# Optimization experiments

Hardware: AMD Instinct MI355X
Metric: run time of the kernel (lower is better)

Reference implementation:

```python
import jax, jax.numpy as jnp
import numpy as np

WS = 8  # window size
NH = 6  # num heads


def _rel_pos_index(ws):
    coords = jnp.stack(jnp.meshgrid(jnp.arange(ws), jnp.arange(ws), indexing='ij'))  # (2, ws, ws)
    cf = coords.reshape(2, -1)                      # (2, ws*ws)
    rel = cf[:, :, None] - cf[:, None, :]           # (2, ws2, ws2)
    return (rel[0] + ws - 1) * (2 * ws - 1) + (rel[1] + ws - 1)  # (ws2, ws2) int


def setup_inputs() -> dict:
    key = jax.random.key(0)
    k1, k2, k3, k4, k5 = jax.random.split(key, 5)
    B, H, W, C = 4, 256, 256, 192
    dim = C
    x = jax.random.normal(k1, (B, H * W, C), dtype=jnp.float32)
    qkv_w = jax.random.normal(k2, (3 * dim, dim), dtype=jnp.float32) * (dim ** -0.5)
    proj_w = jax.random.normal(k3, (dim, dim), dtype=jnp.float32) * (dim ** -0.5)
    proj_b = jax.random.normal(k4, (dim,), dtype=jnp.float32) * 0.01
    rpb_table = jax.random.normal(k5, ((2 * WS - 1) ** 2, NH), dtype=jnp.float32) * 0.02
    return {"x": x, "qkv_w": qkv_w, "proj_w": proj_w, "proj_b": proj_b,
            "rpb_table": rpb_table, "H": H, "W": W}


def reference(x, qkv_w, proj_w, proj_b, rpb_table, H, W):
    B, L, C = x.shape
    ws, nh = WS, NH
    hd = C // nh
    scale = hd ** -0.5
    ws2 = ws * ws

    pad_r = (ws - W % ws) % ws
    pad_b = (ws - H % ws) % ws
    Hp, Wp = H + pad_b, W + pad_r
    xi = x.reshape(B, H, W, C)
    if pad_r > 0 or pad_b > 0:
        xi = jnp.pad(xi, ((0, 0), (0, pad_b), (0, pad_r), (0, 0)))

    # window partition -> (nW, ws2, C)
    win = xi.reshape(B, Hp // ws, ws, Wp // ws, ws, C)
    win = win.transpose(0, 1, 3, 2, 4, 5).reshape(-1, ws2, C)

    # qkv projection (no bias)
    qkv = (win @ qkv_w.T).reshape(-1, ws2, 3, nh, hd)
    q = qkv[:, :, 0].transpose(0, 2, 1, 3) * scale  # (nW, nh, ws2, hd)
    k = qkv[:, :, 1].transpose(0, 2, 1, 3)
    v = qkv[:, :, 2].transpose(0, 2, 1, 3)

    attn = jnp.einsum('nhqd,nhkd->nhqk', q, k)      # (nW, nh, ws2, ws2)
    bias = rpb_table[_rel_pos_index(ws)]            # (ws2, ws2, nh)
    attn = attn + bias.transpose(2, 0, 1)[None]
    attn = jax.nn.softmax(attn, axis=-1)

    out = jnp.einsum('nhqk,nhkd->nhqd', attn, v)    # (nW, nh, ws2, hd)
    out = out.transpose(0, 2, 1, 3).reshape(-1, ws2, C)
    out = out @ proj_w.T + proj_b

    # window reverse
    xo = out.reshape(B, Hp // ws, Wp // ws, ws, ws, C)
    xo = xo.transpose(0, 1, 3, 2, 4, 5).reshape(B, Hp, Wp, C)
    if pad_r > 0 or pad_b > 0:
        xo = xo[:, :H, :W, :]
    return xo.reshape(B, H * W, C)
```

## Files before the change

kernel.cpp:

```cpp
#include <hip/hip_runtime.h>

typedef _Float16 f16;
typedef _Float16 f16x8 __attribute__((ext_vector_type(8)));
typedef _Float16 f16x4 __attribute__((ext_vector_type(4)));
typedef __fp16 h16x2 __attribute__((ext_vector_type(2)));
typedef float f32x4 __attribute__((ext_vector_type(4)));

constexpr int HDIM = 256, WDIM = 256, C_ = 192, NH_ = 6;
constexpr float SCALE = 0.17677669529663687f;
constexpr int XP = 200;

#define SCHED_FENCE() __builtin_amdgcn_sched_barrier(0)

constexpr size_t OFF_WQ   = 0;
constexpr size_t OFF_WP   = 221184;
constexpr size_t OFF_BIAS = 294912;

__global__ __launch_bounds__(256) void prep_kernel(const float* __restrict__ qkv_w,
                                                   const float* __restrict__ proj_w,
                                                   const float* __restrict__ rpb,
                                                   f16* __restrict__ wqp, f16* __restrict__ wpp,
                                                   f16* __restrict__ biasp) {
    int i = blockIdx.x * 256 + threadIdx.x;
    if (i < 13824) {
        int lane = i & 63, rest = i >> 6;
        int ks = rest % 6; rest /= 6;
        int dt = rest & 1; rest >>= 1;
        int c = rest % 3, w = rest / 3;
        int l15 = lane & 15, lg = lane >> 4;
        int row = c * 192 + w * 32 + dt * 16 + l15;
        int col = ks * 32 + lg * 8;
#pragma unroll
        for (int j = 0; j < 8; ++j) wqp[(size_t)i * 8 + j] = (f16)qkv_w[row * 192 + col + j];
    } else if (i < 18432) {
        int g = i - 13824;
        int lane = g & 63, rest = g >> 6;
        int ks = rest % 6; rest /= 6;
        int nt = rest & 1, w = rest >> 1;
        int l15 = lane & 15, lg = lane >> 4;
        int row = w * 32 + nt * 16 + l15;
        int col = ks * 32 + lg * 8;
#pragma unroll
        for (int j = 0; j < 8; ++j) wpp[(size_t)g * 8 + j] = (f16)proj_w[row * 192 + col + j];
    } else if (i < 24576) {
        int g = i - 18432;
        int lane = g & 63;
        int kt = (g >> 6) & 3, qt = (g >> 8) & 3, h = g >> 10;
        int q = qt * 16 + (lane & 15);
#pragma unroll
        for (int j = 0; j < 4; ++j) {
            int k = kt * 16 + (lane >> 4) * 4 + j;
            int dy = (q >> 3) - (k >> 3) + 7;
            int dx = (q & 7) - (k & 7) + 7;
            biasp[(size_t)g * 4 + j] = (f16)rpb[(dy * 15 + dx) * NH_ + h];
        }
    }
}

__global__ __launch_bounds__(128, 2) void fused_kernel(const float* __restrict__ x,
                                                       const f16* __restrict__ wqp,
                                                       const f16* __restrict__ wpp,
                                                       const float* __restrict__ pb,
                                                       const f16* __restrict__ biasp,
                                                       float* __restrict__ out) {
    __shared__ f16 xlds[64 * XP];
    const int tid = threadIdx.x;
    const int v = tid >> 6;
    const int lane = tid & 63;
    const int l15 = lane & 15, lg = lane >> 4;
    const int win = blockIdx.x;
    const int b = win >> 10, wy = (win >> 5) & 31, wx = win & 31;

#pragma unroll
    for (int it = 0; it < 24; ++it) {
        int u = tid + it * 128;
        int row = u / 48, c4 = u - row * 48;
        int gy = wy * 8 + (row >> 3), gx = wx * 8 + (row & 7);
        float4 vv = *((const float4*)(x + ((size_t)((b * HDIM + gy) * WDIM + gx)) * C_ + c4 * 4));
        h16x2 p0 = __builtin_amdgcn_cvt_pkrtz(vv.x, vv.y);
        h16x2 p1 = __builtin_amdgcn_cvt_pkrtz(vv.z, vv.w);
        f16x4 o4;
        o4[0] = (f16)p0[0]; o4[1] = (f16)p0[1]; o4[2] = (f16)p1[0]; o4[3] = (f16)p1[1];
        *((f16x4*)(xlds + row * XP + c4 * 4)) = o4;
    }
    SCHED_FENCE();
    __syncthreads();

    f16x4 oreg[3][4][2];

#pragma unroll
    for (int hh = 0; hh < 3; ++hh) {
        const int head = v * 3 + hh;
        const f16x8* wqb   = (const f16x8*)wqp + (size_t)head * 36 * 64 + lane;
        const f16x4* bbase = (const f16x4*)biasp + (size_t)head * 16 * 64 + lane;
        SCHED_FENCE();

        f16x4 qf[2][4], kf[2][4];
        {
            f32x4 aq[2][4], ak[2][4];
#pragma unroll
            for (int ii = 0; ii < 4; ++ii)
#pragma unroll
                for (int jj = 0; jj < 2; ++jj) {
                    f32x4 z = {0.f, 0.f, 0.f, 0.f};
                    aq[jj][ii] = z; ak[jj][ii] = z;
                }
#pragma unroll
            for (int ks = 0; ks < 6; ++ks) {
                f16x8 Wq0 = wqb[(size_t)(     ks) * 64], Wq1 = wqb[(size_t)( 6 + ks) * 64];
                f16x8 Wk0 = wqb[(size_t)(12 + ks) * 64], Wk1 = wqb[(size_t)(18 + ks) * 64];
#pragma unroll
                for (int tt = 0; tt < 4; ++tt) {
                    f16x8 xt = *((const f16x8*)(xlds + (tt * 16 + l15) * XP + ks * 32 + lg * 8));
                    aq[0][tt] = __builtin_amdgcn_mfma_f32_16x16x32_f16(Wq0, xt, aq[0][tt], 0, 0, 0);
                    aq[1][tt] = __builtin_amdgcn_mfma_f32_16x16x32_f16(Wq1, xt, aq[1][tt], 0, 0, 0);
                    ak[0][tt] = __builtin_amdgcn_mfma_f32_16x16x32_f16(Wk0, xt, ak[0][tt], 0, 0, 0);
                    ak[1][tt] = __builtin_amdgcn_mfma_f32_16x16x32_f16(Wk1, xt, ak[1][tt], 0, 0, 0);
                }
            }
#pragma unroll
            for (int dt = 0; dt < 2; ++dt)
#pragma unroll
                for (int tt = 0; tt < 4; ++tt)
#pragma unroll
                    for (int ii = 0; ii < 4; ++ii) {
                        qf[dt][tt][ii] = (f16)(aq[dt][tt][ii] * SCALE);
                        kf[dt][tt][ii] = (f16)(ak[dt][tt][ii]);
                    }
        }
        SCHED_FENCE();

        f16x4 vf[4][2];
        {
            f32x4 av[4][2];
#pragma unroll
            for (int ii = 0; ii < 4; ++ii)
#pragma unroll
                for (int jj = 0; jj < 2; ++jj) {
                    f32x4 z = {0.f, 0.f, 0.f, 0.f};
                    av[ii][jj] = z;
                }
#pragma unroll
            for (int ks = 0; ks < 6; ++ks) {
                f16x8 Wv0 = wqb[(size_t)(24 + ks) * 64], Wv1 = wqb[(size_t)(30 + ks) * 64];
#pragma unroll
                for (int tt = 0; tt < 4; ++tt) {
                    f16x8 xt = *((const f16x8*)(xlds + (tt * 16 + l15) * XP + ks * 32 + lg * 8));
                    av[tt][0] = __builtin_amdgcn_mfma_f32_16x16x32_f16(xt, Wv0, av[tt][0], 0, 0, 0);
                    av[tt][1] = __builtin_amdgcn_mfma_f32_16x16x32_f16(xt, Wv1, av[tt][1], 0, 0, 0);
                }
            }
#pragma unroll
            for (int tt = 0; tt < 4; ++tt)
#pragma unroll
                for (int dt = 0; dt < 2; ++dt)
#pragma unroll
                    for (int ii = 0; ii < 4; ++ii)
                        vf[tt][dt][ii] = (f16)(av[tt][dt][ii]);
        }
        SCHED_FENCE();

#pragma unroll
        for (int qt = 0; qt < 4; ++qt) {
            f16x4 bq[4];
#pragma unroll
            for (int kt = 0; kt < 4; ++kt)
                bq[kt] = bbase[(size_t)(qt * 4 + kt) * 64];
            f32x4 s[4];
#pragma unroll
            for (int kt = 0; kt < 4; ++kt) {
                f32x4 z = {0.f, 0.f, 0.f, 0.f};
                s[kt] = __builtin_amdgcn_mfma_f32_16x16x16f16(kf[0][kt], qf[0][qt], z, 0, 0, 0);
                s[kt] = __builtin_amdgcn_mfma_f32_16x16x16f16(kf[1][kt], qf[1][qt], s[kt], 0, 0, 0);
            }
#pragma unroll
            for (int kt = 0; kt < 4; ++kt)
#pragma unroll
                for (int ii = 0; ii < 4; ++ii) s[kt][ii] += (float)bq[kt][ii];

            float m = s[0][0];
#pragma unroll
            for (int kt = 0; kt < 4; ++kt)
#pragma unroll
                for (int ii = 0; ii < 4; ++ii) m = fmaxf(m, s[kt][ii]);
            m = fmaxf(m, __shfl_xor(m, 16));
            m = fmaxf(m, __shfl_xor(m, 32));
            float sum = 0.f;
            f16x4 pa[4];
#pragma unroll
            for (int kt = 0; kt < 4; ++kt)
#pragma unroll
                for (int ii = 0; ii < 4; ++ii) {
                    float e = __expf(s[kt][ii] - m);
                    sum += e;
                    pa[kt][ii] = (f16)e;
                }
            sum += __shfl_xor(sum, 16);
            sum += __shfl_xor(sum, 32);
            const float rq = 1.0f / sum;

#pragma unroll
            for (int dt = 0; dt < 2; ++dt) {
                f32x4 z = {0.f, 0.f, 0.f, 0.f};
                f32x4 o0 = __builtin_amdgcn_mfma_f32_16x16x16f16(vf[0][dt], pa[0], z, 0, 0, 0);
                o0 = __builtin_amdgcn_mfma_f32_16x16x16f16(vf[1][dt], pa[1], o0, 0, 0, 0);
                f32x4 o1 = __builtin_amdgcn_mfma_f32_16x16x16f16(vf[2][dt], pa[2], z, 0, 0, 0);
                o1 = __builtin_amdgcn_mfma_f32_16x16x16f16(vf[3][dt], pa[3], o1, 0, 0, 0);
                f32x4 o = o0 + o1;
                f16x4 ov;
#pragma unroll
                for (int ii = 0; ii < 4; ++ii) ov[ii] = (f16)(o[ii] * rq);
                oreg[hh][qt][dt] = ov;
            }
        }
    }
    SCHED_FENCE();
    __syncthreads();

#pragma unroll
    for (int hh = 0; hh < 3; ++hh) {
        const int head = v * 3 + hh;
#pragma unroll
        for (int qt = 0; qt < 4; ++qt)
#pragma unroll
            for (int dt = 0; dt < 2; ++dt)
                *((f16x4*)(xlds + (qt * 16 + l15) * XP + head * 32 + dt * 16 + lg * 4)) = oreg[hh][qt][dt];
    }
    SCHED_FENCE();
    __syncthreads();

#pragma unroll
    for (int hh = 0; hh < 3; ++hh) {
        const int head = v * 3 + hh;
        const f16x8* wpb = (const f16x8*)wpp + (size_t)head * 12 * 64 + lane;
#pragma unroll
        for (int nt = 0; nt < 2; ++nt) {
            f16x8 wpf[6];
#pragma unroll
            for (int ks = 0; ks < 6; ++ks)
                wpf[ks] = wpb[(size_t)(nt * 6 + ks) * 64];
            f32x4 bv = *((const f32x4*)(pb + head * 32 + nt * 16 + lg * 4));
#pragma unroll
            for (int qt = 0; qt < 4; ++qt) {
                f32x4 acc = {0.f, 0.f, 0.f, 0.f};
#pragma unroll
                for (int ks = 0; ks < 6; ++ks) {
                    f16x8 af = *((const f16x8*)(xlds + (qt * 16 + l15) * XP + ks * 32 + lg * 8));
                    acc = __builtin_amdgcn_mfma_f32_16x16x32_f16(wpf[ks], af, acc, 0, 0, 0);
                }
                acc += bv;
                const int t = qt * 16 + l15;
                const int gy = wy * 8 + (t >> 3), gx = wx * 8 + (t & 7);
                *((f32x4*)(out + ((size_t)((b * HDIM + gy) * WDIM + gx)) * C_ + head * 32 + nt * 16 + lg * 4)) = acc;
            }
        }
    }
}

extern "C" void kernel_launch(void* const* d_in, const int* in_sizes, int n_in,
                              void* d_out, int out_size, void* d_ws, size_t ws_size,
                              hipStream_t stream) {
    const float* x      = (const float*)d_in[0];
    const float* qkv_w  = (const float*)d_in[1];
    const float* proj_w = (const float*)d_in[2];
    const float* proj_b = (const float*)d_in[3];
    const float* rpb    = (const float*)d_in[4];
    float* out = (float*)d_out;
    char* ws = (char*)d_ws;
    f16* wqp   = (f16*)(ws + OFF_WQ);
    f16* wpp   = (f16*)(ws + OFF_WP);
    f16* biasp = (f16*)(ws + OFF_BIAS);

    prep_kernel<<<96, 256, 0, stream>>>(qkv_w, proj_w, rpb, wqp, wpp, biasp);
    fused_kernel<<<4096, 128, 0, stream>>>(x, wqp, wpp, proj_b, biasp, out);
}
```

Before: 172.6 us.

## Split Q/K projection, raise occupancy, use exp2 with folded log2e scaling

Splits the fused Q and K projection loops into separate phases so fewer accumulators are live at once, and raises launch bounds to 3 blocks per CU to allow more waves. Folds log2(e) into the query scale and the relative-position bias so softmax can use raw v_exp_f32 (base-2) via inline asm, and replaces the division with a hardware reciprocal. The x load loop is broken into three scheduling groups. Risks include register spills under the tighter budget and slightly lower precision from the approximate reciprocal.

```diff
diff --git a/kernel.cpp b/kernel.cpp
--- a/kernel.cpp
+++ b/kernel.cpp
@@ -8,6 +8,8 @@
 
 constexpr int HDIM = 256, WDIM = 256, C_ = 192, NH_ = 6;
 constexpr float SCALE = 0.17677669529663687f;
+constexpr float L2E = 1.4426950408889634f;
+constexpr float SCALE2 = SCALE * L2E;
 constexpr int XP = 200;
 
 #define SCHED_FENCE() __builtin_amdgcn_sched_barrier(0)
@@ -52,12 +54,12 @@
             int k = kt * 16 + (lane >> 4) * 4 + j;
             int dy = (q >> 3) - (k >> 3) + 7;
             int dx = (q & 7) - (k & 7) + 7;
-            biasp[(size_t)g * 4 + j] = (f16)rpb[(dy * 15 + dx) * NH_ + h];
+            biasp[(size_t)g * 4 + j] = (f16)(rpb[(dy * 15 + dx) * NH_ + h] * L2E);
         }
     }
 }
 
-__global__ __launch_bounds__(128, 2) void fused_kernel(const float* __restrict__ x,
+__global__ __launch_bounds__(128, 3) void fused_kernel(const float* __restrict__ x,
                                                        const f16* __restrict__ wqp,
                                                        const f16* __restrict__ wpp,
                                                        const float* __restrict__ pb,
@@ -72,18 +74,21 @@
     const int b = win >> 10, wy = (win >> 5) & 31, wx = win & 31;
 
 #pragma unroll
-    for (int it = 0; it < 24; ++it) {
-        int u = tid + it * 128;
-        int row = u / 48, c4 = u - row * 48;
-        int gy = wy * 8 + (row >> 3), gx = wx * 8 + (row & 7);
-        float4 vv = *((const float4*)(x + ((size_t)((b * HDIM + gy) * WDIM + gx)) * C_ + c4 * 4));
-        h16x2 p0 = __builtin_amdgcn_cvt_pkrtz(vv.x, vv.y);
-        h16x2 p1 = __builtin_amdgcn_cvt_pkrtz(vv.z, vv.w);
-        f16x4 o4;
-        o4[0] = (f16)p0[0]; o4[1] = (f16)p0[1]; o4[2] = (f16)p1[0]; o4[3] = (f16)p1[1];
-        *((f16x4*)(xlds + row * XP + c4 * 4)) = o4;
-    }
-    SCHED_FENCE();
+    for (int grp = 0; grp < 3; ++grp) {
+#pragma unroll
+        for (int it8 = 0; it8 < 8; ++it8) {
+            int u = tid + (grp * 8 + it8) * 128;
+            int row = u / 48, c4 = u - row * 48;
+            int gy = wy * 8 + (row >> 3), gx = wx * 8 + (row & 7);
+            float4 vv = *((const float4*)(x + ((size_t)((b * HDIM + gy) * WDIM + gx)) * C_ + c4 * 4));
+            h16x2 p0 = __builtin_amdgcn_cvt_pkrtz(vv.x, vv.y);
+            h16x2 p1 = __builtin_amdgcn_cvt_pkrtz(vv.z, vv.w);
+            f16x4 o4;
+            o4[0] = (f16)p0[0]; o4[1] = (f16)p0[1]; o4[2] = (f16)p1[0]; o4[3] = (f16)p1[1];
+            *((f16x4*)(xlds + row * XP + c4 * 4)) = o4;
+        }
+        SCHED_FENCE();
+    }
     __syncthreads();
 
     f16x4 oreg[3][4][2];
@@ -95,27 +100,21 @@
         const f16x4* bbase = (const f16x4*)biasp + (size_t)head * 16 * 64 + lane;
         SCHED_FENCE();
 
-        f16x4 qf[2][4], kf[2][4];
+        f16x4 qf[2][4];
         {
-            f32x4 aq[2][4], ak[2][4];
+            f32x4 aq[2][4];
 #pragma unroll
             for (int ii = 0; ii < 4; ++ii)
 #pragma unroll
-                for (int jj = 0; jj < 2; ++jj) {
-                    f32x4 z = {0.f, 0.f, 0.f, 0.f};
-                    aq[jj][ii] = z; ak[jj][ii] = z;
-                }
+                for (int jj = 0; jj < 2; ++jj) { f32x4 z = {0.f,0.f,0.f,0.f}; aq[jj][ii] = z; }
 #pragma unroll
             for (int ks = 0; ks < 6; ++ks) {
-                f16x8 Wq0 = wqb[(size_t)(     ks) * 64], Wq1 = wqb[(size_t)( 6 + ks) * 64];
-                f16x8 Wk0 = wqb[(size_t)(12 + ks) * 64], Wk1 = wqb[(size_t)(18 + ks) * 64];
+                f16x8 W0 = wqb[(size_t)(ks) * 64], W1 = wqb[(size_t)(6 + ks) * 64];
 #pragma unroll
                 for (int tt = 0; tt < 4; ++tt) {
                     f16x8 xt = *((const f16x8*)(xlds + (tt * 16 + l15) * XP + ks * 32 + lg * 8));
-                    aq[0][tt] = __builtin_amdgcn_mfma_f32_16x16x32_f16(Wq0, xt, aq[0][tt], 0, 0, 0);
-                    aq[1][tt] = __builtin_amdgcn_mfma_f32_16x16x32_f16(Wq1, xt, aq[1][tt], 0, 0, 0);
-                    ak[0][tt] = __builtin_amdgcn_mfma_f32_16x16x32_f16(Wk0, xt, ak[0][tt], 0, 0, 0);
-                    ak[1][tt] = __builtin_amdgcn_mfma_f32_16x16x32_f16(Wk1, xt, ak[1][tt], 0, 0, 0);
+                    aq[0][tt] = __builtin_amdgcn_mfma_f32_16x16x32_f16(W0, xt, aq[0][tt], 0, 0, 0);
+                    aq[1][tt] = __builtin_amdgcn_mfma_f32_16x16x32_f16(W1, xt, aq[1][tt], 0, 0, 0);
                 }
             }
 #pragma unroll
@@ -123,10 +122,35 @@
 #pragma unroll
                 for (int tt = 0; tt < 4; ++tt)
 #pragma unroll
-                    for (int ii = 0; ii < 4; ++ii) {
-                        qf[dt][tt][ii] = (f16)(aq[dt][tt][ii] * SCALE);
+                    for (int ii = 0; ii < 4; ++ii)
+                        qf[dt][tt][ii] = (f16)(aq[dt][tt][ii] * SCALE2);
+        }
+        SCHED_FENCE();
+
+        f16x4 kf[2][4];
+        {
+            f32x4 ak[2][4];
+#pragma unroll
+            for (int ii = 0; ii < 4; ++ii)
+#pragma unroll
+                for (int jj = 0; jj < 2; ++jj) { f32x4 z = {0.f,0.f,0.f,0.f}; ak[jj][ii] = z; }
+#pragma unroll
+            for (int ks = 0; ks < 6; ++ks) {
+                f16x8 W0 = wqb[(size_t)(12 + ks) * 64], W1 = wqb[(size_t)(18 + ks) * 64];
+#pragma unroll
+                for (int tt = 0; tt < 4; ++tt) {
+                    f16x8 xt = *((const f16x8*)(xlds + (tt * 16 + l15) * XP + ks * 32 + lg * 8));
+                    ak[0][tt] = __builtin_amdgcn_mfma_f32_16x16x32_f16(W0, xt, ak[0][tt], 0, 0, 0);
+                    ak[1][tt] = __builtin_amdgcn_mfma_f32_16x16x32_f16(W1, xt, ak[1][tt], 0, 0, 0);
+                }
+            }
+#pragma unroll
+            for (int dt = 0; dt < 2; ++dt)
+#pragma unroll
+                for (int tt = 0; tt < 4; ++tt)
+#pragma unroll
+                    for (int ii = 0; ii < 4; ++ii)
                         kf[dt][tt][ii] = (f16)(ak[dt][tt][ii]);
-                    }
         }
         SCHED_FENCE();
 
@@ -136,18 +160,15 @@
 #pragma unroll
             for (int ii = 0; ii < 4; ++ii)
 #pragma unroll
-                for (int jj = 0; jj < 2; ++jj) {
-                    f32x4 z = {0.f, 0.f, 0.f, 0.f};
-                    av[ii][jj] = z;
-                }
+                for (int jj = 0; jj < 2; ++jj) { f32x4 z = {0.f,0.f,0.f,0.f}; av[ii][jj] = z; }
 #pragma unroll
             for (int ks = 0; ks < 6; ++ks) {
-                f16x8 Wv0 = wqb[(size_t)(24 + ks) * 64], Wv1 = wqb[(size_t)(30 + ks) * 64];
+                f16x8 W0 = wqb[(size_t)(24 + ks) * 64], W1 = wqb[(size_t)(30 + ks) * 64];
 #pragma unroll
                 for (int tt = 0; tt < 4; ++tt) {
                     f16x8 xt = *((const f16x8*)(xlds + (tt * 16 + l15) * XP + ks * 32 + lg * 8));
-                    av[tt][0] = __builtin_amdgcn_mfma_f32_16x16x32_f16(xt, Wv0, av[tt][0], 0, 0, 0);
-                    av[tt][1] = __builtin_amdgcn_mfma_f32_16x16x32_f16(xt, Wv1, av[tt][1], 0, 0, 0);
+                    av[tt][0] = __builtin_amdgcn_mfma_f32_16x16x32_f16(xt, W0, av[tt][0], 0, 0, 0);
+                    av[tt][1] = __builtin_amdgcn_mfma_f32_16x16x32_f16(xt, W1, av[tt][1], 0, 0, 0);
                 }
             }
 #pragma unroll
@@ -191,13 +212,14 @@
             for (int kt = 0; kt < 4; ++kt)
 #pragma unroll
                 for (int ii = 0; ii < 4; ++ii) {
-                    float e = __expf(s[kt][ii] - m);
+                    float e;
+                    asm("v_exp_f32 %0, %1" : "=v"(e) : "v"(s[kt][ii] - m));
                     sum += e;
                     pa[kt][ii] = (f16)e;
                 }
             sum += __shfl_xor(sum, 16);
             sum += __shfl_xor(sum, 32);
-            const float rq = 1.0f / sum;
+            const float rq = __builtin_amdgcn_rcpf(sum);
 
 #pragma unroll
             for (int dt = 0; dt < 2; ++dt) {
```

Result: no change. 173.6 us (+0.6%).
